# Kernel tuning notes

Hardware: AMD Instinct MI355X
Metric: run time of the kernel (lower is better)

Reference implementation:

```python
import jax, jax.numpy as jnp
import numpy as np

B, N, D = 4, 4096, 128
R, K, O = 4, 16, 128


def setup_inputs() -> dict:
    key = jax.random.key(0)
    k1, k2, k3, k4 = jax.random.split(key, 4)
    node_features = jax.random.normal(k1, (B, N, D), dtype=jnp.float32)
    # index 0 selects the zero-pad row; valid node i is index i+1
    neighbor_indices = jax.random.randint(k2, (B, R, N, K), 0, N + 1, dtype=jnp.int32)
    relation_kernels = jax.random.normal(k3, (R, D, O), dtype=jnp.float32) * (1.0 / np.sqrt(D))
    self_kernel = jax.random.normal(k4, (D, O), dtype=jnp.float32) * (1.0 / np.sqrt(D))
    bias = jnp.zeros((O,), dtype=jnp.float32)
    return {
        "node_features": node_features,
        "neighbor_indices": neighbor_indices,
        "relation_kernels": relation_kernels,
        "self_kernel": self_kernel,
        "bias": bias,
    }


def reference(node_features, neighbor_indices, relation_kernels, self_kernel, bias):
    b, n, d = node_features.shape
    # prepend zero row so index 0 acts as padding (matches tf.concat zero_pad)
    padded = jnp.concatenate(
        [jnp.zeros((b, 1, d), node_features.dtype), node_features], axis=1
    )  # [B, N+1, D]
    # batched gather (tf.gather batch_dims=1): [B, R, N, K, D]
    neighbor_features = jax.vmap(lambda p, i: p[i])(padded, neighbor_indices)
    aggregated = neighbor_features.mean(axis=3)  # [B, R, N, D]
    # per-relation matmul then sum over relations
    total_msg = jnp.einsum("brnd,rdo->bno", aggregated, relation_kernels)
    self_msg = jnp.einsum("bnd,do->bno", node_features, self_kernel)
    out = total_msg + self_msg + bias
    return jax.nn.relu(out)  # dropout is identity at inference (rate=0.0)
```

## Files before the change

### kernel.cpp

```cpp
#include <hip/hip_runtime.h>
#include <cstddef>

namespace {
constexpr int B_ = 4, N_ = 4096, D_ = 128, R_ = 4, K_ = 16, O_ = 128;
constexpr int NP1 = N_ + 1;
constexpr int TN = 16;
constexpr int THREADS = 512;
constexpr int KK = (R_ + 1) * D_;
constexpr int PITCH_A = KK + 8;
}

typedef __bf16 bf16x8 __attribute__((ext_vector_type(8)));
typedef __bf16 bf16x4 __attribute__((ext_vector_type(4)));
typedef __bf16 bf16x2 __attribute__((ext_vector_type(2)));
typedef float  f32x4v __attribute__((ext_vector_type(4)));
using u32 = unsigned int;

__global__ __launch_bounds__(256)
void prep_all(const float* __restrict__ nf, const float* __restrict__ relk,
              const float* __restrict__ selfk,
              __bf16* __restrict__ ptab, __bf16* __restrict__ wt) {
    int t = blockIdx.x * 256 + threadIdx.x;
    const int total_tab = B_ * NP1 * (D_ / 4);
    if (t < total_tab) {
        const int b   = t / (NP1 * 32);
        const int rem = t % (NP1 * 32);
        const int row = rem >> 5;
        const int q   = rem & 31;
        bf16x4 res;
        if (row == 0) {
            res[0] = (__bf16)0.f; res[1] = (__bf16)0.f;
            res[2] = (__bf16)0.f; res[3] = (__bf16)0.f;
        } else {
            const float4 v = *(const float4*)(nf + ((size_t)b * N_ + (row - 1)) * D_ + q * 4);
            res[0] = (__bf16)v.x; res[1] = (__bf16)v.y;
            res[2] = (__bf16)v.z; res[3] = (__bf16)v.w;
        }
        *(bf16x4*)(ptab + ((size_t)b * NP1 + row) * D_ + q * 4) = res;
        return;
    }
    t -= total_tab;
    if (t < O_ * (KK / 4)) {
        const int o   = t / (KK / 4);
        const int kk  = (t % (KK / 4)) * 4;
        bf16x4 res;
        #pragma unroll
        for (int i = 0; i < 4; ++i) {
            const int kki = kk + i;
            const float w = (kki < R_ * D_) ? relk[(size_t)kki * O_ + o]
                                            : selfk[(size_t)(kki - R_ * D_) * O_ + o];
            res[i] = (__bf16)w;
        }
        *(bf16x4*)(wt + (size_t)o * KK + kk) = res;
    }
}

__global__ __launch_bounds__(THREADS, 8)
void gcn_fused(const __bf16* __restrict__ ptab,
               const int*    __restrict__ nbr,
               const __bf16* __restrict__ wt,
               const float*  __restrict__ bias,
               float*        __restrict__ out)
{
    __shared__ __bf16 agg[TN][PITCH_A];

    const int hw   = blockIdx.x;
    const int xcd  = hw & 7;
    const int b    = xcd >> 1;
    const int tile = (xcd & 1) + ((hw >> 3) << 1);
    const int n0   = tile * TN;

    const int tid = threadIdx.x;
    const int wv  = tid >> 6;
    const int l   = tid & 63;

    {
        const int r  = wv & 3;
        const int nb = (wv >> 2) * 8;
        const int ioff = __builtin_amdgcn_readfirstlane(
            (((b * R_ + r) * N_) + n0 + nb) * K_);
        const int* __restrict__ ib = nbr + ioff;
        const __bf16* __restrict__ tb = ptab + (size_t)b * NP1 * D_;

        #pragma unroll 2
        for (int n = 0; n < 8; ++n) {
            int sidx[K_];
            #pragma unroll
            for (int k = 0; k < K_; ++k) sidx[k] = ib[n * K_ + k];

            float acl[4] = {0.f, 0.f, 0.f, 0.f};
            float ach[4] = {0.f, 0.f, 0.f, 0.f};
            #pragma unroll
            for (int k = 0; k < K_; ++k) {
                const u32 u = *((const u32*)(tb + (size_t)sidx[k] * D_) + l);
                acl[k & 3] += __uint_as_float(u << 16);
                ach[k & 3] += __uint_as_float(u & 0xffff0000u);
            }
            const float lo = (acl[0] + acl[1]) + (acl[2] + acl[3]);
            const float hi = (ach[0] + ach[1]) + (ach[2] + ach[3]);
            bf16x2 res;
            res[0] = (__bf16)(lo * 0.0625f);
            res[1] = (__bf16)(hi * 0.0625f);
            *(bf16x2*)&agg[nb + n][r * D_ + l * 2] = res;
        }

        #pragma unroll
        for (int j = 0; j < 2; ++j) {
            const int n = wv * 2 + j;
            const u32 u = *((const u32*)(ptab + ((size_t)b * NP1 + n0 + n + 1) * D_) + l);
            *((u32*)&agg[n][R_ * D_] + l) = u;
        }
    }
    __syncthreads();

    const int lr = l & 15;
    const int lk = l >> 4;
    const int ct = wv;

    const __bf16* __restrict__ wr = wt + (size_t)(ct * 16 + lr) * KK + lk * 8;
    const __bf16* arow = &agg[lr][lk * 8];

    f32x4v acc = {0.f, 0.f, 0.f, 0.f};
    #pragma unroll 5
    for (int k0 = 0; k0 < KK; k0 += 32) {
        const bf16x8 a  = *(const bf16x8*)(arow + k0);
        const bf16x8 bf = *(const bf16x8*)(wr + k0);
        acc = __builtin_amdgcn_mfma_f32_16x16x32_bf16(a, bf, acc, 0, 0, 0);
    }

    const float bv = bias[ct * 16 + lr];
    #pragma unroll
    for (int j = 0; j < 4; ++j) {
        const int row = lk * 4 + j;
        out[((size_t)b * N_ + n0 + row) * O_ + ct * 16 + lr] = fmaxf(acc[j] + bv, 0.f);
    }
}

extern "C" void kernel_launch(void* const* d_in, const int* in_sizes, int n_in,
                              void* d_out, int out_size, void* d_ws, size_t ws_size,
                              hipStream_t stream) {
    const float* nf    = (const float*)d_in[0];
    const int*   nbr   = (const int*)  d_in[1];
    const float* relk  = (const float*)d_in[2];
    const float* selfk = (const float*)d_in[3];
    const float* bias  = (const float*)d_in[4];
    float* outp = (float*)d_out;

    __bf16* ptab = (__bf16*)d_ws;
    __bf16* wtp  = (__bf16*)((char*)d_ws + (size_t)B_ * NP1 * D_ * 2);

    {
        const int total = B_ * NP1 * (D_ / 4) + O_ * (KK / 4);
        prep_all<<<(total + 255) / 256, 256, 0, stream>>>(nf, relk, selfk, ptab, wtp);
    }

    dim3 grid(B_ * (N_ / TN));
    gcn_fused<<<grid, THREADS, 0, stream>>>(ptab, nbr, wtp, bias, outp);
}
```

Before: 39.21 us.

## Split fused gather+GEMM into separate gather and GEMM kernels via global buffer

The single fused kernel is replaced by a gather kernel that writes bf16 neighbor sums to a global workspace and a separate MFMA GEMM kernel that reads them plus the self features. The mean's 1/16 factor is folded into the relation weights during prep. Each GEMM wave now computes two 16-row tiles to reuse weight loads. The aim is to decouple the latency-bound gather from the GEMM and remove the block-wide barrier, at the cost of an extra kernel launch and a global round trip for the aggregated features.

```diff
diff --git a/kernel.cpp b/kernel.cpp
--- a/kernel.cpp
+++ b/kernel.cpp
@@ -4,16 +4,15 @@
 namespace {
 constexpr int B_ = 4, N_ = 4096, D_ = 128, R_ = 4, K_ = 16, O_ = 128;
 constexpr int NP1 = N_ + 1;
-constexpr int TN = 16;
-constexpr int THREADS = 512;
 constexpr int KK = (R_ + 1) * D_;
-constexpr int PITCH_A = KK + 8;
+constexpr int KR = R_ * D_;
 }
 
 typedef __bf16 bf16x8 __attribute__((ext_vector_type(8)));
 typedef __bf16 bf16x4 __attribute__((ext_vector_type(4)));
 typedef __bf16 bf16x2 __attribute__((ext_vector_type(2)));
 typedef float  f32x4v __attribute__((ext_vector_type(4)));
+typedef float  f32x2v __attribute__((ext_vector_type(2)));
 using u32 = unsigned int;
 
 __global__ __launch_bounds__(256)
@@ -47,92 +46,102 @@
         #pragma unroll
         for (int i = 0; i < 4; ++i) {
             const int kki = kk + i;
-            const float w = (kki < R_ * D_) ? relk[(size_t)kki * O_ + o]
-                                            : selfk[(size_t)(kki - R_ * D_) * O_ + o];
+            const float w = (kki < KR) ? relk[(size_t)kki * O_ + o] * 0.0625f
+                                       : selfk[(size_t)(kki - KR) * O_ + o];
             res[i] = (__bf16)w;
         }
         *(bf16x4*)(wt + (size_t)o * KK + kk) = res;
     }
 }
 
-__global__ __launch_bounds__(THREADS, 8)
-void gcn_fused(const __bf16* __restrict__ ptab,
-               const int*    __restrict__ nbr,
-               const __bf16* __restrict__ wt,
-               const float*  __restrict__ bias,
-               float*        __restrict__ out)
+__global__ __launch_bounds__(256, 8)
+void gcn_gather(const __bf16* __restrict__ ptab, const int* __restrict__ nbr,
+                __bf16* __restrict__ aggw)
 {
-    __shared__ __bf16 agg[TN][PITCH_A];
+    const int hw  = blockIdx.x;
+    const int xcd = hw & 7;
+    const int b   = xcd >> 1;
+    const int lb  = ((hw >> 3) << 1) | (xcd & 1);
+    const int wv  = threadIdx.x >> 6;
+    const int l   = threadIdx.x & 63;
+    const int n0  = lb * 4;
 
-    const int hw   = blockIdx.x;
-    const int xcd  = hw & 7;
-    const int b    = xcd >> 1;
-    const int tile = (xcd & 1) + ((hw >> 3) << 1);
-    const int n0   = tile * TN;
+    const __bf16* __restrict__ tb = ptab + (size_t)b * NP1 * D_;
+    const int ioff = __builtin_amdgcn_readfirstlane((((b * R_ + wv) * N_) + n0) * K_);
+    const int* __restrict__ ib = nbr + ioff;
 
-    const int tid = threadIdx.x;
-    const int wv  = tid >> 6;
-    const int l   = tid & 63;
+    #pragma unroll 2
+    for (int n = 0; n < 4; ++n) {
+        int sidx[K_];
+        #pragma unroll
+        for (int k = 0; k < K_; ++k) sidx[k] = ib[n * K_ + k];
 
-    {
-        const int r  = wv & 3;
-        const int nb = (wv >> 2) * 8;
-        const int ioff = __builtin_amdgcn_readfirstlane(
-            (((b * R_ + r) * N_) + n0 + nb) * K_);
-        const int* __restrict__ ib = nbr + ioff;
-        const __bf16* __restrict__ tb = ptab + (size_t)b * NP1 * D_;
+        f32x2v a0 = {0.f, 0.f}, a1 = {0.f, 0.f}, a2 = {0.f, 0.f}, a3 = {0.f, 0.f};
+        #pragma unroll
+        for (int k = 0; k < K_; ++k) {
+            const u32 u = *((const u32*)(tb + (size_t)sidx[k] * D_) + l);
+            f32x2v v;
+            v.x = __uint_as_float(u << 16);
+            v.y = __uint_as_float(u & 0xffff0000u);
+            switch (k & 3) {
+                case 0:  a0 += v; break;
+                case 1:  a1 += v; break;
+                case 2:  a2 += v; break;
+                default: a3 += v; break;
+            }
+        }
+        const f32x2v s = (a0 + a1) + (a2 + a3);
+        bf16x2 res;
+        res[0] = (__bf16)s.x;
+        res[1] = (__bf16)s.y;
+        *(bf16x2*)(aggw + ((size_t)(b * N_ + n0 + n)) * KR + wv * D_ + l * 2) = res;
+    }
+}
 
-        #pragma unroll 2
-        for (int n = 0; n < 8; ++n) {
-            int sidx[K_];
-            #pragma unroll
-            for (int k = 0; k < K_; ++k) sidx[k] = ib[n * K_ + k];
-
-            float acl[4] = {0.f, 0.f, 0.f, 0.f};
-            float ach[4] = {0.f, 0.f, 0.f, 0.f};
-            #pragma unroll
-            for (int k = 0; k < K_; ++k) {
-                const u32 u = *((const u32*)(tb + (size_t)sidx[k] * D_) + l);
-                acl[k & 3] += __uint_as_float(u << 16);
-                ach[k & 3] += __uint_as_float(u & 0xffff0000u);
-            }
-            const float lo = (acl[0] + acl[1]) + (acl[2] + acl[3]);
-            const float hi = (ach[0] + ach[1]) + (ach[2] + ach[3]);
-            bf16x2 res;
-            res[0] = (__bf16)(lo * 0.0625f);
-            res[1] = (__bf16)(hi * 0.0625f);
-            *(bf16x2*)&agg[nb + n][r * D_ + l * 2] = res;
-        }
-
-        #pragma unroll
-        for (int j = 0; j < 2; ++j) {
-            const int n = wv * 2 + j;
-            const u32 u = *((const u32*)(ptab + ((size_t)b * NP1 + n0 + n + 1) * D_) + l);
-            *((u32*)&agg[n][R_ * D_] + l) = u;
-        }
-    }
-    __syncthreads();
-
+__global__ __launch_bounds__(512, 8)
+void gcn_gemm(const __bf16* __restrict__ aggw, const __bf16* __restrict__ ptab,
+              const __bf16* __restrict__ wt, const float* __restrict__ bias,
+              float* __restrict__ out)
+{
+    const int hw = blockIdx.x;
+    const int b  = hw >> 7;
+    const int n0 = (hw & 127) * 32;
+    const int wv = threadIdx.x >> 6;
+    const int l  = threadIdx.x & 63;
     const int lr = l & 15;
     const int lk = l >> 4;
-    const int ct = wv;
 
-    const __bf16* __restrict__ wr = wt + (size_t)(ct * 16 + lr) * KK + lk * 8;
-    const __bf16* arow = &agg[lr][lk * 8];
+    const __bf16* __restrict__ wr  = wt + (size_t)(wv * 16 + lr) * KK + lk * 8;
+    const __bf16* __restrict__ ar0 = aggw + (size_t)(b * N_ + n0 + lr) * KR + lk * 8;
+    const __bf16* __restrict__ ar1 = ar0 + 16 * KR;
+    const __bf16* __restrict__ sp0 = ptab + ((size_t)b * NP1 + n0 + lr + 1) * D_ + lk * 8;
+    const __bf16* __restrict__ sp1 = sp0 + 16 * D_;
 
-    f32x4v acc = {0.f, 0.f, 0.f, 0.f};
-    #pragma unroll 5
-    for (int k0 = 0; k0 < KK; k0 += 32) {
-        const bf16x8 a  = *(const bf16x8*)(arow + k0);
-        const bf16x8 bf = *(const bf16x8*)(wr + k0);
-        acc = __builtin_amdgcn_mfma_f32_16x16x32_bf16(a, bf, acc, 0, 0, 0);
+    f32x4v acc0 = {0.f, 0.f, 0.f, 0.f};
+    f32x4v acc1 = {0.f, 0.f, 0.f, 0.f};
+    #pragma unroll 4
+    for (int k0 = 0; k0 < KR; k0 += 32) {
+        const bf16x8 w  = *(const bf16x8*)(wr + k0);
+        const bf16x8 a0 = *(const bf16x8*)(ar0 + k0);
+        const bf16x8 a1 = *(const bf16x8*)(ar1 + k0);
+        acc0 = __builtin_amdgcn_mfma_f32_16x16x32_bf16(a0, w, acc0, 0, 0, 0);
+        acc1 = __builtin_amdgcn_mfma_f32_16x16x32_bf16(a1, w, acc1, 0, 0, 0);
+    }
+    #pragma unroll
+    for (int k0 = 0; k0 < D_; k0 += 32) {
+        const bf16x8 w  = *(const bf16x8*)(wr + KR + k0);
+        const bf16x8 a0 = *(const bf16x8*)(sp0 + k0);
+        const bf16x8 a1 = *(const bf16x8*)(sp1 + k0);
+        acc0 = __builtin_amdgcn_mfma_f32_16x16x32_bf16(a0, w, acc0, 0, 0, 0);
+        acc1 = __builtin_amdgcn_mfma_f32_16x16x32_bf16(a1, w, acc1, 0, 0, 0);
     }
 
-    const float bv = bias[ct * 16 + lr];
+    const float bv = bias[wv * 16 + lr];
     #pragma unroll
     for (int j = 0; j < 4; ++j) {
-        const int row = lk * 4 + j;
-        out[((size_t)b * N_ + n0 + row) * O_ + ct * 16 + lr] = fmaxf(acc[j] + bv, 0.f);
+        const int row0 = n0 + lk * 4 + j;
+        out[((size_t)b * N_ + row0) * O_ + wv * 16 + lr]      = fmaxf(acc0[j] + bv, 0.f);
+        out[((size_t)b * N_ + row0 + 16) * O_ + wv * 16 + lr] = fmaxf(acc1[j] + bv, 0.f);
     }
 }
 
@@ -147,13 +156,13 @@
     float* outp = (float*)d_out;
 
     __bf16* ptab = (__bf16*)d_ws;
-    __bf16* wtp  = (__bf16*)((char*)d_ws + (size_t)B_ * NP1 * D_ * 2);
+    __bf16* wtp  = ptab + (size_t)B_ * NP1 * D_;
+    __bf16* aggw = wtp + (size_t)O_ * KK;
 
     {
         const int total = B_ * NP1 * (D_ / 4) + O_ * (KK / 4);
         prep_all<<<(total + 255) / 256, 256, 0, stream>>>(nf, relk, selfk, ptab, wtp);
     }
-
-    dim3 grid(B_ * (N_ / TN));
-    gcn_fused<<<grid, THREADS, 0, stream>>>(ptab, nbr, wtp, bias, outp);
+    gcn_gather<<<4096, 256, 0, stream>>>(ptab, nbr, aggw);
+    gcn_gemm<<<512, 512, 0, stream>>>(aggw, ptab, wtp, bias, outp);
 }
```

Result: slower. 57.70 us (+47.2%).

## Gather neighbor features from an FP8 table with half-wave neighbor split

Applied to the files above, without the earlier changes.

Adds an FP8 (e4m3) copy of the padded node table, built in the prep kernel, and gathers neighbor rows from it instead of the bf16 table. Each half-wave handles alternate neighbors over a full 128-byte row, and the halves are combined with a cross-lane shuffle before writing bf16 aggregates to shared memory. The aim is to halve the bytes moved by the random gather, which dominates cost. In exchange the prep kernel writes an extra table, and the aggregated features carry FP8 quantization error, which may exceed the accuracy tolerance.

```diff
diff --git a/kernel.cpp b/kernel.cpp
--- a/kernel.cpp
+++ b/kernel.cpp
@@ -12,14 +12,15 @@
 
 typedef __bf16 bf16x8 __attribute__((ext_vector_type(8)));
 typedef __bf16 bf16x4 __attribute__((ext_vector_type(4)));
-typedef __bf16 bf16x2 __attribute__((ext_vector_type(2)));
 typedef float  f32x4v __attribute__((ext_vector_type(4)));
+typedef float  f32x2v __attribute__((ext_vector_type(2)));
 using u32 = unsigned int;
 
 __global__ __launch_bounds__(256)
 void prep_all(const float* __restrict__ nf, const float* __restrict__ relk,
               const float* __restrict__ selfk,
-              __bf16* __restrict__ ptab, __bf16* __restrict__ wt) {
+              __bf16* __restrict__ ptab, unsigned char* __restrict__ ptab8,
+              __bf16* __restrict__ wt) {
     int t = blockIdx.x * 256 + threadIdx.x;
     const int total_tab = B_ * NP1 * (D_ / 4);
     if (t < total_tab) {
@@ -40,6 +41,21 @@
         return;
     }
     t -= total_tab;
+    if (t < total_tab) {
+        const int b   = t / (NP1 * 32);
+        const int rem = t % (NP1 * 32);
+        const int row = rem >> 5;
+        const int q   = rem & 31;
+        u32 v8 = 0u;
+        if (row != 0) {
+            const float4 v = *(const float4*)(nf + ((size_t)b * N_ + (row - 1)) * D_ + q * 4);
+            v8 = (u32)__builtin_amdgcn_cvt_pk_fp8_f32(v.x, v.y, 0, false);
+            v8 = (u32)__builtin_amdgcn_cvt_pk_fp8_f32(v.z, v.w, (int)v8, true);
+        }
+        *(u32*)(ptab8 + ((size_t)b * NP1 + row) * D_ + q * 4) = v8;
+        return;
+    }
+    t -= total_tab;
     if (t < O_ * (KK / 4)) {
         const int o   = t / (KK / 4);
         const int kk  = (t % (KK / 4)) * 4;
@@ -57,6 +73,7 @@
 
 __global__ __launch_bounds__(THREADS, 8)
 void gcn_fused(const __bf16* __restrict__ ptab,
+               const unsigned char* __restrict__ ptab8,
                const int*    __restrict__ nbr,
                const __bf16* __restrict__ wt,
                const float*  __restrict__ bias,
@@ -73,6 +90,8 @@
     const int tid = threadIdx.x;
     const int wv  = tid >> 6;
     const int l   = tid & 63;
+    const int l31 = l & 31;
+    const bool hiHalf = (l & 32) != 0;
 
     {
         const int r  = wv & 3;
@@ -80,7 +99,7 @@
         const int ioff = __builtin_amdgcn_readfirstlane(
             (((b * R_ + r) * N_) + n0 + nb) * K_);
         const int* __restrict__ ib = nbr + ioff;
-        const __bf16* __restrict__ tb = ptab + (size_t)b * NP1 * D_;
+        const unsigned char* __restrict__ tb8 = ptab8 + (size_t)b * NP1 * D_;
 
         #pragma unroll 2
         for (int n = 0; n < 8; ++n) {
@@ -88,20 +107,31 @@
             #pragma unroll
             for (int k = 0; k < K_; ++k) sidx[k] = ib[n * K_ + k];
 
-            float acl[4] = {0.f, 0.f, 0.f, 0.f};
-            float ach[4] = {0.f, 0.f, 0.f, 0.f};
+            f32x2v e0a = {0.f, 0.f}, e0b = {0.f, 0.f};
+            f32x2v e1a = {0.f, 0.f}, e1b = {0.f, 0.f};
             #pragma unroll
-            for (int k = 0; k < K_; ++k) {
-                const u32 u = *((const u32*)(tb + (size_t)sidx[k] * D_) + l);
-                acl[k & 3] += __uint_as_float(u << 16);
-                ach[k & 3] += __uint_as_float(u & 0xffff0000u);
+            for (int p = 0; p < 8; ++p) {
+                const int idx = hiHalf ? sidx[2 * p + 1] : sidx[2 * p];
+                const u32 u = *(const u32*)(tb8 + (size_t)idx * D_ + l31 * 4);
+                const f32x2v v0 = __builtin_amdgcn_cvt_pk_f32_fp8(u, false);
+                const f32x2v v1 = __builtin_amdgcn_cvt_pk_f32_fp8(u, true);
+                if (p & 1) { e0b += v0; e1b += v1; }
+                else       { e0a += v0; e1a += v1; }
             }
-            const float lo = (acl[0] + acl[1]) + (acl[2] + acl[3]);
-            const float hi = (ach[0] + ach[1]) + (ach[2] + ach[3]);
-            bf16x2 res;
-            res[0] = (__bf16)(lo * 0.0625f);
-            res[1] = (__bf16)(hi * 0.0625f);
-            *(bf16x2*)&agg[nb + n][r * D_ + l * 2] = res;
+            f32x2v e0 = e0a + e0b;
+            f32x2v e1 = e1a + e1b;
+            e0.x += __shfl_xor(e0.x, 32, 64);
+            e0.y += __shfl_xor(e0.y, 32, 64);
+            e1.x += __shfl_xor(e1.x, 32, 64);
+            e1.y += __shfl_xor(e1.y, 32, 64);
+            if (!hiHalf) {
+                bf16x4 res;
+                res[0] = (__bf16)(e0.x * 0.0625f);
+                res[1] = (__bf16)(e0.y * 0.0625f);
+                res[2] = (__bf16)(e1.x * 0.0625f);
+                res[3] = (__bf16)(e1.y * 0.0625f);
+                *(bf16x4*)&agg[nb + n][r * D_ + l31 * 4] = res;
+            }
         }
 
         #pragma unroll
@@ -147,13 +177,15 @@
     float* outp = (float*)d_out;
 
     __bf16* ptab = (__bf16*)d_ws;
-    __bf16* wtp  = (__bf16*)((char*)d_ws + (size_t)B_ * NP1 * D_ * 2);
+    __bf16* wtp  = ptab + (size_t)B_ * NP1 * D_;
+    unsigned char* ptab8 = (unsigned char*)(wtp + (size_t)O_ * KK);
 
     {
-        const int total = B_ * NP1 * (D_ / 4) + O_ * (KK / 4);
-        prep_all<<<(total + 255) / 256, 256, 0, stream>>>(nf, relk, selfk, ptab, wtp);
+        const int total = 2 * B_ * NP1 * (D_ / 4) + O_ * (KK / 4);
+        prep_all<<<(total + 255) / 256, 256, 0, stream>>>(nf, relk, selfk,
+                                                          ptab, ptab8, wtp);
     }
 
     dim3 grid(B_ * (N_ / TN));
-    gcn_fused<<<grid, THREADS, 0, stream>>>(ptab, nbr, wtp, bias, outp);
+    gcn_fused<<<grid, THREADS, 0, stream>>>(ptab, ptab8, nbr, wtp, bias, outp);
 }
```

New measurement: 67.98 us. 73.4% more time.
